# Kernel optimization log

Measured on AMD Instinct MI355X. Metric: run time of the kernel, lower is better.

The kernel has to match this reference:

```python
import jax, jax.numpy as jnp
import numpy as np

STRIDE, PAD, DIL = 1, 1, 1  # from init_kwargs
RELU = True


def setup_inputs() -> dict:
    key = jax.random.key(0)
    k1, k2, k3 = jax.random.split(key, 3)
    B, Cin, Cout, H, W, K = 32, 128, 256, 56, 56, 3
    # uint8 quantized codes stored as float32 (module does .float() before conv)
    x = jnp.round(jax.random.uniform(k1, (B, Cin, H, W), dtype=jnp.float32) * 255.0)
    weight = jnp.round(jax.random.uniform(k2, (Cout, Cin, K, K), dtype=jnp.float32) * 255.0)
    # int32 quantized bias (scale = s_x * s_w, zero_point = 0)
    bias = jnp.round(jax.random.normal(k3, (Cout,), dtype=jnp.float32) * 1000.0)
    return {
        "x": x,
        "weight": weight,
        "bias": bias,
        "M": jnp.float32(0.0021),      # s_x * s_w / s_y
        "x_zero": jnp.float32(128.0),
        "w_zero": jnp.float32(127.0),
        "y_zero": jnp.float32(0.0),
    }


def reference(x, weight, bias, M, x_zero, w_zero, y_zero):
    # x: [B, Cin, H, W] uint8 codes as float; weight: [Cout, Cin, kh, kw]
    xz = x - x_zero                    # zero-point sub (padding adds literal 0s, as in torch: pad AFTER sub)
    w = weight - w_zero
    y = jax.lax.conv_general_dilated(
        xz, w,
        window_strides=(STRIDE, STRIDE),
        padding=((PAD, PAD), (PAD, PAD)),
        rhs_dilation=(DIL, DIL),
        dimension_numbers=("NCHW", "OIHW", "NCHW"),
    )
    y = (y + bias[None, :, None, None]) * M + y_zero  # requantize
    if RELU:
        y = jnp.maximum(y, y_zero)     # clamp below at output zero-point
    return jnp.round(y)
```

## Files before the change

kernel.cpp:

```cpp
#include <hip/hip_runtime.h>
#include <hip/hip_bf16.h>


typedef __attribute__((ext_vector_type(4))) int   i32x4;
typedef __attribute__((ext_vector_type(4))) float f32x4;

#define WTI8_BYTES (18 * 16384)
#define XPI8_BYTES (32 * 58 * 8192)

__device__ __forceinline__ void gload_lds16(const void* g, void* l) {
    __builtin_amdgcn_global_load_lds(
        (const __attribute__((address_space(1))) void*)g,
        (__attribute__((address_space(3))) void*)l, 16, 0, 0);
}

__global__ void prep_kernel(const float* __restrict__ x, const float* __restrict__ xzp,
                            const float* __restrict__ w,
                            char* __restrict__ xpi8, int* __restrict__ colsum,
                            char* __restrict__ wt) {
    int tid = threadIdx.x;
    if (blockIdx.x >= 32 * 58) {
        int cidx = (blockIdx.x - 32 * 58) * 256 + tid;
        int byte0 = cidx * 16;
        int s    = byte0 >> 14;
        int wn   = (byte0 >> 12) & 3;
        int e4   = byte0 & 4095;
        int nn   = e4 >> 6;
        int koff = e4 & 63;
        int kl   = koff ^ ((nn & 3) << 4);
        int n = wn * 64 + nn;
        int r = s >> 1, ch = s & 1;
        union { char c[16]; i32x4 v; } u;
#pragma unroll
        for (int j = 0; j < 16; ++j) {
            int cin = ch * 64 + kl + j;
            u.c[j] = (char)((int)w[(size_t)n * 1152 + cin * 9 + r] - 128);
        }
        *(i32x4*)(wt + byte0) = u.v;
        return;
    }
    int bhh = blockIdx.x;
    int b = bhh / 58, hh = bhh % 58;
    char* blob = xpi8 + (size_t)bhh * 8192;
    int wcol = tid & 63;
    int cq = tid >> 6;
    __shared__ int ps[4][64];
    if (hh == 0 || hh == 57) {
        i32x4 z = {0, 0, 0, 0};
        *(i32x4*)(blob + tid * 32)      = z;
        *(i32x4*)(blob + tid * 32 + 16) = z;
        if (cq == 0) colsum[bhh * 64 + wcol] = 0;
        return;
    }
    const int ZX = (int)rintf(*xzp);
    bool valid = (wcol >= 1 && wcol <= 56);
    const float* xb = x + (size_t)b * 128 * 3136 + (size_t)(hh - 1) * 56 +
                      (valid ? (wcol - 1) : 0);
    int csum = 0;
#pragma unroll
    for (int u = 0; u < 2; ++u) {
        union { char c[16]; i32x4 v; } uu;
#pragma unroll
        for (int j = 0; j < 16; ++j) {
            int c = cq * 32 + u * 16 + j;
            int val = valid ? ((int)xb[(size_t)c * 3136] - ZX) : 0;
            uu.c[j] = (char)val;
            csum += val;
        }
        *(i32x4*)(blob + wcol * 128 + ((cq * 32 + u * 16) ^ ((wcol & 7) << 4))) = uu.v;
    }
    ps[cq][wcol] = csum;
    __syncthreads();
    if (cq == 0)
        colsum[bhh * 64 + wcol] = ps[0][wcol] + ps[1][wcol] + ps[2][wcol] + ps[3][wcol];
}

__global__ __launch_bounds__(256, 2)
void conv_kernel(const char* __restrict__ wt,
                 const char* __restrict__ xpi8,
                 const int* __restrict__ colsum,
                 const float* __restrict__ bias,
                 const float* __restrict__ Mp,
                 const float* __restrict__ wzp,
                 const float* __restrict__ yzp,
                 float* __restrict__ out) {
    __shared__ __align__(1024) char As[32768];
    __shared__ __align__(1024) char Bp[32768];
    __shared__ int s2row[2][64];

    const int tid = threadIdx.x;
    const int lane = tid & 63;
    const int wn = tid >> 6;
    const int l15 = lane & 15, lg = lane >> 4;
    const int bx = (blockIdx.x % 8) * 112 + (blockIdx.x / 8);
    const int b = bx / 28;
    const int h0 = (bx % 28) * 2;

    char* bpriv = Bp + wn * 8192;
    const char* bwsrc = wt + wn * 4096 + lane * 16;
    const int bfoff = (lg * 16) ^ ((l15 & 3) << 4);

    const char* agbase = xpi8 + (size_t)(b * 58 + h0) * 8192;
#pragma unroll
    for (int i = 0; i < 8; ++i)
        gload_lds16(agbase + i * 4096 + tid * 16, As + i * 4096 + tid * 16);
#pragma unroll
    for (int st = 0; st < 2; ++st)
#pragma unroll
        for (int i = 0; i < 4; ++i)
            gload_lds16(bwsrc + (size_t)st * 16384 + i * 1024,
                        bpriv + st * 4096 + i * 1024 + lane * 16);
    if (tid < 128) {
        int row = tid >> 6, m = tid & 63;
        int s = 0;
        if (m < 56) {
#pragma unroll
            for (int kh = 0; kh < 3; ++kh)
#pragma unroll
                for (int kw = 0; kw < 3; ++kw)
                    s += colsum[(b * 58 + h0 + row + kh) * 64 + m + kw];
        }
        s2row[row][m] = s;
    }

    i32x4 acc[4][8];
#pragma unroll
    for (int i = 0; i < 4; ++i)
#pragma unroll
        for (int j = 0; j < 8; ++j)
            acc[i][j] = (i32x4){0, 0, 0, 0};

    __syncthreads();

#pragma unroll
    for (int s = 0; s < 18; ++s) {
        const int kh = (s >> 1) / 3, kw = (s >> 1) % 3, ch = s & 1;
        const char* bslot = bpriv + (s & 1) * 4096;
        i32x4 bfr[4];
#pragma unroll
        for (int fn = 0; fn < 4; ++fn)
            bfr[fn] = *(const i32x4*)(bslot + (fn * 16 + l15) * 64 + bfoff);
        i32x4 afr[8];
#pragma unroll
        for (int fm = 0; fm < 8; ++fm) {
            int rowoff = fm >> 2;
            int wv = (fm & 3) * 16 + l15 + kw;
            int wc = wv > 63 ? 63 : wv;
            int ab = (rowoff + kh) * 8192 + wc * 128 +
                     ((ch * 64 + lg * 16) ^ ((wc & 7) << 4));
            afr[fm] = *(const i32x4*)(As + ab);
        }
        if (s < 16) {
            asm volatile("s_waitcnt lgkmcnt(0)" ::: "memory");
#pragma unroll
            for (int i = 0; i < 4; ++i)
                gload_lds16(bwsrc + (size_t)(s + 2) * 16384 + i * 1024,
                            bpriv + (s & 1) * 4096 + i * 1024 + lane * 16);
            asm volatile("s_waitcnt vmcnt(4)" ::: "memory");
        } else if (s == 16) {
            asm volatile("s_waitcnt vmcnt(0)" ::: "memory");
        }
        __builtin_amdgcn_s_setprio(1);
#pragma unroll
        for (int fn = 0; fn < 4; ++fn)
#pragma unroll
            for (int fm = 0; fm < 8; ++fm)
                acc[fn][fm] = __builtin_amdgcn_mfma_i32_16x16x64_i8(
                    bfr[fn], afr[fm], acc[fn][fm], 0, 0, 0);
        __builtin_amdgcn_s_setprio(0);
    }

    const float Mv  = *Mp;
    const float yzv = *yzp;
    const float CWf = 128.0f - *wzp;
#pragma unroll
    for (int fn = 0; fn < 4; ++fn) {
#pragma unroll
        for (int reg = 0; reg < 4; ++reg) {
            const int cout = wn * 64 + fn * 16 + lg * 4 + reg;
            const float bv = bias[cout];
#pragma unroll
            for (int fm = 0; fm < 8; ++fm) {
                const int row = fm >> 2;
                const int m = (fm & 3) * 16 + l15;
                if (m < 56) {
                    const size_t rowb =
                        ((size_t)(b * 256 + cout) * 56 + h0 + row) * 56;
                    float af = (float)acc[fn][fm][reg] +
                               CWf * (float)s2row[row][m];
                    float v = (af + bv) * Mv + yzv;
                    v = fmaxf(v, yzv);
                    out[rowb + m] = rintf(v);
                }
            }
        }
    }
}

extern "C" void kernel_launch(void* const* d_in, const int* in_sizes, int n_in,
                              void* d_out, int out_size, void* d_ws, size_t ws_size,
                              hipStream_t stream) {
    const float* x    = (const float*)d_in[0];
    const float* w    = (const float*)d_in[1];
    const float* bias = (const float*)d_in[2];
    const float* Mp   = (const float*)d_in[3];
    const float* xzp  = (const float*)d_in[4];
    const float* wzp  = (const float*)d_in[5];
    const float* yzp  = (const float*)d_in[6];
    float* out = (float*)d_out;

    char* wt     = (char*)d_ws;
    char* xpi8   = wt + WTI8_BYTES;
    int*  colsum = (int*)(xpi8 + XPI8_BYTES);

    prep_kernel<<<32 * 58 + 72, 256, 0, stream>>>(x, xzp, w, xpi8, colsum, wt);
    conv_kernel<<<32 * 28, 256, 0, stream>>>(wt, xpi8, colsum, bias, Mp, wzp, yzp, out);
}
```

Measured before the change: 69.40 us.

## Process two row tiles per block and overlap next tile loads with epilogue

Each conv block now handles four output rows as two sequential two-row tiles, so the grid is halved. The activation, weight and column-sum loads for the second tile are issued before the first tile's epilogue stores, so loads and stores can overlap. The per-block reads of the requant scalars are hoisted out of the epilogue. The cost is fewer blocks than the resident slots can hold, so some of them sit idle, plus a longer serial path per block.

```diff
diff --git a/kernel.cpp b/kernel.cpp
--- a/kernel.cpp
+++ b/kernel.cpp
@@ -75,6 +75,76 @@
         colsum[bhh * 64 + wcol] = ps[0][wcol] + ps[1][wcol] + ps[2][wcol] + ps[3][wcol];
 }
 
+__device__ __forceinline__ void kloop(const char* As, char* bpriv,
+                                      const char* bwsrc, int lane,
+                                      int l15, int lg, int bfoff,
+                                      i32x4 acc[4][8]) {
+#pragma unroll
+    for (int s = 0; s < 18; ++s) {
+        const int kh = (s >> 1) / 3, kw = (s >> 1) % 3, ch = s & 1;
+        const char* bslot = bpriv + (s & 1) * 4096;
+        i32x4 bfr[4];
+#pragma unroll
+        for (int fn = 0; fn < 4; ++fn)
+            bfr[fn] = *(const i32x4*)(bslot + (fn * 16 + l15) * 64 + bfoff);
+        i32x4 afr[8];
+#pragma unroll
+        for (int fm = 0; fm < 8; ++fm) {
+            int rowoff = fm >> 2;
+            int wv = (fm & 3) * 16 + l15 + kw;
+            int wc = wv > 63 ? 63 : wv;
+            int ab = (rowoff + kh) * 8192 + wc * 128 +
+                     ((ch * 64 + lg * 16) ^ ((wc & 7) << 4));
+            afr[fm] = *(const i32x4*)(As + ab);
+        }
+        if (s < 16) {
+            asm volatile("s_waitcnt lgkmcnt(0)" ::: "memory");
+#pragma unroll
+            for (int i = 0; i < 4; ++i)
+                gload_lds16(bwsrc + (size_t)(s + 2) * 16384 + i * 1024,
+                            bpriv + (s & 1) * 4096 + i * 1024 + lane * 16);
+            asm volatile("s_waitcnt vmcnt(4)" ::: "memory");
+        } else if (s == 16) {
+            asm volatile("s_waitcnt vmcnt(0)" ::: "memory");
+        }
+        __builtin_amdgcn_s_setprio(1);
+#pragma unroll
+        for (int fn = 0; fn < 4; ++fn)
+#pragma unroll
+            for (int fm = 0; fm < 8; ++fm)
+                acc[fn][fm] = __builtin_amdgcn_mfma_i32_16x16x64_i8(
+                    bfr[fn], afr[fm], acc[fn][fm], 0, 0, 0);
+        __builtin_amdgcn_s_setprio(0);
+    }
+}
+
+__device__ __forceinline__ void epilogue(const i32x4 acc[4][8], const int s2t[2][64],
+                                         const float* bias, float Mv, float yzv,
+                                         float CWf, int wn, int l15, int lg,
+                                         int b, int h0, float* out) {
+#pragma unroll
+    for (int fn = 0; fn < 4; ++fn) {
+#pragma unroll
+        for (int reg = 0; reg < 4; ++reg) {
+            const int cout = wn * 64 + fn * 16 + lg * 4 + reg;
+            const float bv = bias[cout];
+#pragma unroll
+            for (int fm = 0; fm < 8; ++fm) {
+                const int row = fm >> 2;
+                const int m = (fm & 3) * 16 + l15;
+                if (m < 56) {
+                    const size_t rowb =
+                        ((size_t)(b * 256 + cout) * 56 + h0 + row) * 56;
+                    float af = (float)acc[fn][fm][reg] + CWf * (float)s2t[row][m];
+                    float v = (af + bv) * Mv + yzv;
+                    v = fmaxf(v, yzv);
+                    out[rowb + m] = rintf(v);
+                }
+            }
+        }
+    }
+}
+
 __global__ __launch_bounds__(256, 2)
 void conv_kernel(const char* __restrict__ wt,
                  const char* __restrict__ xpi8,
@@ -86,24 +156,28 @@
                  float* __restrict__ out) {
     __shared__ __align__(1024) char As[32768];
     __shared__ __align__(1024) char Bp[32768];
-    __shared__ int s2row[2][64];
+    __shared__ int s2row[2][2][64];
 
     const int tid = threadIdx.x;
     const int lane = tid & 63;
     const int wn = tid >> 6;
     const int l15 = lane & 15, lg = lane >> 4;
-    const int bx = (blockIdx.x % 8) * 112 + (blockIdx.x / 8);
-    const int b = bx / 28;
-    const int h0 = (bx % 28) * 2;
+    const int bx = (blockIdx.x % 8) * 56 + (blockIdx.x / 8);
+    const int b = bx / 14;
+    const int h0 = (bx % 14) * 4;
 
     char* bpriv = Bp + wn * 8192;
     const char* bwsrc = wt + wn * 4096 + lane * 16;
     const int bfoff = (lg * 16) ^ ((l15 & 3) << 4);
 
-    const char* agbase = xpi8 + (size_t)(b * 58 + h0) * 8192;
+    const float Mv  = *Mp;
+    const float yzv = *yzp;
+    const float CWf = 128.0f - *wzp;
+
+    const char* ag0 = xpi8 + (size_t)(b * 58 + h0) * 8192;
 #pragma unroll
     for (int i = 0; i < 8; ++i)
-        gload_lds16(agbase + i * 4096 + tid * 16, As + i * 4096 + tid * 16);
+        gload_lds16(ag0 + i * 4096 + tid * 16, As + i * 4096 + tid * 16);
 #pragma unroll
     for (int st = 0; st < 2; ++st)
 #pragma unroll
@@ -120,7 +194,7 @@
                 for (int kw = 0; kw < 3; ++kw)
                     s += colsum[(b * 58 + h0 + row + kh) * 64 + m + kw];
         }
-        s2row[row][m] = s;
+        s2row[0][row][m] = s;
     }
 
     i32x4 acc[4][8];
@@ -132,69 +206,46 @@
 
     __syncthreads();
 
-#pragma unroll
-    for (int s = 0; s < 18; ++s) {
-        const int kh = (s >> 1) / 3, kw = (s >> 1) % 3, ch = s & 1;
-        const char* bslot = bpriv + (s & 1) * 4096;
-        i32x4 bfr[4];
-#pragma unroll
-        for (int fn = 0; fn < 4; ++fn)
-            bfr[fn] = *(const i32x4*)(bslot + (fn * 16 + l15) * 64 + bfoff);
-        i32x4 afr[8];
-#pragma unroll
-        for (int fm = 0; fm < 8; ++fm) {
-            int rowoff = fm >> 2;
-            int wv = (fm & 3) * 16 + l15 + kw;
-            int wc = wv > 63 ? 63 : wv;
-            int ab = (rowoff + kh) * 8192 + wc * 128 +
-                     ((ch * 64 + lg * 16) ^ ((wc & 7) << 4));
-            afr[fm] = *(const i32x4*)(As + ab);
-        }
-        if (s < 16) {
-            asm volatile("s_waitcnt lgkmcnt(0)" ::: "memory");
-#pragma unroll
-            for (int i = 0; i < 4; ++i)
-                gload_lds16(bwsrc + (size_t)(s + 2) * 16384 + i * 1024,
-                            bpriv + (s & 1) * 4096 + i * 1024 + lane * 16);
-            asm volatile("s_waitcnt vmcnt(4)" ::: "memory");
-        } else if (s == 16) {
-            asm volatile("s_waitcnt vmcnt(0)" ::: "memory");
-        }
-        __builtin_amdgcn_s_setprio(1);
-#pragma unroll
-        for (int fn = 0; fn < 4; ++fn)
-#pragma unroll
-            for (int fm = 0; fm < 8; ++fm)
-                acc[fn][fm] = __builtin_amdgcn_mfma_i32_16x16x64_i8(
-                    bfr[fn], afr[fm], acc[fn][fm], 0, 0, 0);
-        __builtin_amdgcn_s_setprio(0);
-    }
-
-    const float Mv  = *Mp;
-    const float yzv = *yzp;
-    const float CWf = 128.0f - *wzp;
-#pragma unroll
-    for (int fn = 0; fn < 4; ++fn) {
-#pragma unroll
-        for (int reg = 0; reg < 4; ++reg) {
-            const int cout = wn * 64 + fn * 16 + lg * 4 + reg;
-            const float bv = bias[cout];
-#pragma unroll
-            for (int fm = 0; fm < 8; ++fm) {
-                const int row = fm >> 2;
-                const int m = (fm & 3) * 16 + l15;
-                if (m < 56) {
-                    const size_t rowb =
-                        ((size_t)(b * 256 + cout) * 56 + h0 + row) * 56;
-                    float af = (float)acc[fn][fm][reg] +
-                               CWf * (float)s2row[row][m];
-                    float v = (af + bv) * Mv + yzv;
-                    v = fmaxf(v, yzv);
-                    out[rowb + m] = rintf(v);
-                }
-            }
-        }
-    }
+    kloop(As, bpriv, bwsrc, lane, l15, lg, bfoff, acc);
+
+    __syncthreads();
+
+    const char* ag1 = xpi8 + (size_t)(b * 58 + h0 + 2) * 8192;
+#pragma unroll
+    for (int i = 0; i < 8; ++i)
+        gload_lds16(ag1 + i * 4096 + tid * 16, As + i * 4096 + tid * 16);
+#pragma unroll
+    for (int st = 0; st < 2; ++st)
+#pragma unroll
+        for (int i = 0; i < 4; ++i)
+            gload_lds16(bwsrc + (size_t)st * 16384 + i * 1024,
+                        bpriv + st * 4096 + i * 1024 + lane * 16);
+    if (tid < 128) {
+        int row = tid >> 6, m = tid & 63;
+        int s = 0;
+        if (m < 56) {
+#pragma unroll
+            for (int kh = 0; kh < 3; ++kh)
+#pragma unroll
+                for (int kw = 0; kw < 3; ++kw)
+                    s += colsum[(b * 58 + h0 + 2 + row + kh) * 64 + m + kw];
+        }
+        s2row[1][row][m] = s;
+    }
+
+    epilogue(acc, s2row[0], bias, Mv, yzv, CWf, wn, l15, lg, b, h0, out);
+
+    __syncthreads();
+
+#pragma unroll
+    for (int i = 0; i < 4; ++i)
+#pragma unroll
+        for (int j = 0; j < 8; ++j)
+            acc[i][j] = (i32x4){0, 0, 0, 0};
+
+    kloop(As, bpriv, bwsrc, lane, l15, lg, bfoff, acc);
+
+    epilogue(acc, s2row[1], bias, Mv, yzv, CWf, wn, l15, lg, b, h0 + 2, out);
 }
 
 extern "C" void kernel_launch(void* const* d_in, const int* in_sizes, int n_in,
@@ -214,5 +265,5 @@
     int*  colsum = (int*)(xpi8 + XPI8_BYTES);
 
     prep_kernel<<<32 * 58 + 72, 256, 0, stream>>>(x, xzp, w, xpi8, colsum, wt);
-    conv_kernel<<<32 * 28, 256, 0, stream>>>(wt, xpi8, colsum, bias, Mp, wzp, yzp, out);
-}
+    conv_kernel<<<32 * 14, 256, 0, stream>>>(wt, xpi8, colsum, bias, Mp, wzp, yzp, out);
+}
```

Measured after the change: 94.98 us. 1.37x slower.
